# Kernel optimization log

Hardware: AMD Instinct MI355X
Metric: run time of the kernel (lower is better)

## Reference

```python
import jax, jax.numpy as jnp
import numpy as np

N, K, D, H, F = 4, 2048, 512, 8, 2048
Dh = D // H  # per-head dim_q = dim_v = dim_out = 64
EPS = 1e-10


def _uinit(k, shape, fan_sum):
    c = (6.0 / fan_sum) ** 0.5
    return jax.random.uniform(k, shape, jnp.float32, -c, c)


def setup_inputs() -> dict:
    key = jax.random.key(0)
    ks = jax.random.split(key, 8)
    x = jax.random.normal(ks[0], (N, K, D), jnp.float32)
    # per-head projection weights, stacked over heads: (H, D, Dh)
    Wq = _uinit(ks[1], (H, D, Dh), D + Dh)
    Wk = _uinit(ks[2], (H, D, Dh), D + Dh)
    Wv = _uinit(ks[3], (H, D, Dh), D + Dh)
    bq = jnp.zeros((H, Dh), jnp.float32)
    bk = jnp.zeros((H, Dh), jnp.float32)
    bv = jnp.zeros((H, Dh), jnp.float32)
    Wo = _uinit(ks[4], (H * Dh, D), H * Dh + D)
    bo = jnp.zeros((D,), jnp.float32)
    W1 = _uinit(ks[5], (D, F), D + F)
    b1 = jnp.zeros((F,), jnp.float32)
    W2 = _uinit(ks[6], (F, D), F + D)
    b2 = jnp.zeros((D,), jnp.float32)
    g1 = jnp.ones((D,), jnp.float32)
    be1 = jnp.zeros((D,), jnp.float32)
    g2 = jnp.ones((D,), jnp.float32)
    be2 = jnp.zeros((D,), jnp.float32)
    # causal mask: True = masked position (masked_fill semantics)
    mask = jnp.broadcast_to(jnp.triu(jnp.ones((K, K), bool), 1), (N, K, K))
    return dict(x=x, Wq=Wq, bq=bq, Wk=Wk, bk=bk, Wv=Wv, bv=bv, Wo=Wo, bo=bo,
                W1=W1, b1=b1, W2=W2, b2=b2, g1=g1, be1=be1, g2=g2, be2=be2,
                mask=mask)


def _layer_norm(x, g, b):
    m = x.mean(-1, keepdims=True)
    v = ((x - m) ** 2).mean(-1, keepdims=True)
    return g * (x - m) / jnp.sqrt(v + EPS) + b


def _block(x, Wq, bq, Wk, bk, Wv, bv, Wo, bo, W1, b1, W2, b2, g1, be1, g2, be2, mask):
    # per-head projections: (N, H, K, Dh)
    q = jnp.einsum('nkd,hde->nhke', x, Wq) + bq[None, :, None, :]
    k = jnp.einsum('nkd,hde->nhke', x, Wk) + bk[None, :, None, :]
    v = jnp.einsum('nkd,hde->nhke', x, Wv) + bv[None, :, None, :]
    # full score matrix (N, H, K, K) -- faithful to bmm-softmax-bmm
    s = jnp.einsum('nhqe,nhke->nhqk', q, k) / (Dh ** 0.5)
    s = jnp.where(mask[:, None], -1e9, s)
    w = jax.nn.softmax(s, axis=-1)
    att = jnp.einsum('nhqk,nhke->nhqe', w, v)
    att = att.transpose(0, 2, 1, 3).reshape(N, K, H * Dh)  # concat heads
    att = att @ Wo + bo
    h1 = _layer_norm(x + att, g1, be1)
    ff = jax.nn.relu(h1 @ W1 + b1) @ W2 + b2
    return _layer_norm(h1 + ff, g2, be2)


def reference(x, Wq, bq, Wk, bk, Wv, bv, Wo, bo, W1, b1, W2, b2, g1, be1, g2, be2, mask):
    return _block(x, Wq, bq, Wk, bk, Wv, bv, Wo, bo, W1, b1, W2, b2, g1, be1, g2, be2, mask)
```

## Files before the change

### kernel.cpp

```cpp
#include <hip/hip_runtime.h>
#include <cstdint>

typedef unsigned short u16;
typedef __bf16 bf16x8 __attribute__((ext_vector_type(8)));
typedef float f32x4 __attribute__((ext_vector_type(4)));
struct __align__(8) U2 { unsigned x, y; };

#define NEG_INF (-__builtin_inff())

__device__ __forceinline__ u16 f2bf(float f) {
  unsigned u = __builtin_bit_cast(unsigned, f);
  u += 0x7FFFu + ((u >> 16) & 1u);
  return (u16)(u >> 16);
}
__device__ __forceinline__ float bf2f(u16 b) {
  unsigned u = (unsigned)b << 16;
  return __builtin_bit_cast(float, u);
}
__device__ __forceinline__ u16 bfbits(__bf16 x) { return __builtin_bit_cast(u16, x); }
__device__ __forceinline__ unsigned pk2(float a, float b) {
  u16 lo = bfbits((__bf16)a), hi = bfbits((__bf16)b);
  return (unsigned)lo | ((unsigned)hi << 16);
}

__device__ __forceinline__ void async16(u16* dst, const u16* src) {
  __builtin_amdgcn_global_load_lds(
      (__attribute__((address_space(1))) void*)(u16*)src,
      (__attribute__((address_space(3))) void*)dst, 16, 0, 0);
}

__global__ __launch_bounds__(256) void k_cvt(const float4* __restrict__ in,
                                             uint4* __restrict__ out, int n8) {
  int i = blockIdx.x * 256 + threadIdx.x;
  if (i >= n8) return;
  float4 a = in[2 * i], b = in[2 * i + 1];
  uint4 r;
  r.x = (unsigned)f2bf(a.x) | ((unsigned)f2bf(a.y) << 16);
  r.y = (unsigned)f2bf(a.z) | ((unsigned)f2bf(a.w) << 16);
  r.z = (unsigned)f2bf(b.x) | ((unsigned)f2bf(b.y) << 16);
  r.w = (unsigned)f2bf(b.z) | ((unsigned)f2bf(b.w) << 16);
  out[i] = r;
}

__global__ __launch_bounds__(256) void k_prep(const float* __restrict__ Wo,
                                              const float* __restrict__ W1,
                                              const float* __restrict__ W2,
                                              const float* __restrict__ Wq,
                                              const float* __restrict__ Wk,
                                              const float* __restrict__ Wv,
                                              const float* __restrict__ bq,
                                              const float* __restrict__ bk,
                                              const float* __restrict__ bv,
                                              u16* __restrict__ WoT,
                                              u16* __restrict__ W1T,
                                              u16* __restrict__ W2T,
                                              u16* __restrict__ WqkvT,
                                              float* __restrict__ bqkv) {
  const int b = blockIdx.x, tid = threadIdx.x;
  if (b >= 1536) {
    int i = (b - 1536) * 256 + tid;
    int m = i >> 9, r = i & 511;
    const float* B = (m == 0) ? bq : (m == 1) ? bk : bv;
    bqkv[i] = B[r];
    return;
  }
  __shared__ float t[32][65];
  const float* ip;
  u16* op;
  int R, C, r0, c0;
  if (b < 128)      { ip = Wo; op = WoT; R = 512;  C = 512;  c0 = (b & 7) * 64;          r0 = (b >> 3) * 32; }
  else if (b < 640) { int i = b - 128; ip = W1; op = W1T; R = 512;  C = 2048; c0 = (i & 31) * 64; r0 = (i >> 5) * 32; }
  else if (b < 1152){ int i = b - 640; ip = W2; op = W2T; R = 2048; C = 512;  c0 = (i & 7) * 64;  r0 = (i >> 3) * 32; }
  else {
    int i = b - 1152;
    int z = i >> 4;
    const float* W = (z < 8) ? Wq : (z < 16) ? Wk : Wv;
    ip = W + (size_t)(z & 7) * 32768;
    op = WqkvT + (size_t)z * 32768;
    R = 512; C = 64; c0 = 0; r0 = (i & 15) * 32;
  }
  int tx = tid & 63, ty = tid >> 6;
#pragma unroll
  for (int i = 0; i < 32; i += 4)
    t[ty + i][tx] = ip[(size_t)(r0 + ty + i) * C + c0 + tx];
  __syncthreads();
  int cx = tid & 31, cy = tid >> 5;
#pragma unroll
  for (int j = 0; j < 64; j += 8)
    op[(size_t)(c0 + cy + j) * R + r0 + cx] = f2bf(t[cx][cy + j]);
}

template <bool DBUF, int EPI, int BN>
__global__ __launch_bounds__(256) void k_gemm(const u16* __restrict__ A,
                                              const u16* __restrict__ BT,
                                              const float* __restrict__ bias,
                                              u16* __restrict__ Cout,
                                              int M, int N, int Kd) {
  constexpr int HALF = 8192 + BN * 64;
  __shared__ __align__(16) u16 lds[DBUF ? 2 * HALF : HALF];
  constexpr int NFR = BN / 32;
  constexpr int BITER = BN / 32;
  const int tid = threadIdx.x, wid = tid >> 6, lane = tid & 63;
  const int lr = lane & 15, lg = lane >> 4;
  const int wr = wid >> 1, wc = wid & 1;
  const int bid = blockIdx.x;
  const int xcd = bid & 7, local = bid >> 3;
  const int tm = (xcd * 8 + (local & 7)) * 128;
  const int tn = (local >> 3) * BN;

  f32x4 acc[4][NFR] = {};

  const int srow = lane >> 3;
  const int kb = (lane & 7) ^ srow;

  auto STAGE = [&](int buf, int kt) {
    u16* base = lds + buf * HALF;
#pragma unroll
    for (int it = 0; it < 4; ++it) {
      int rid = wid * 4 + it;
      int row = rid * 8 + srow;
      async16(base + rid * 512, A + (size_t)(tm + row) * Kd + kt + kb * 8);
    }
#pragma unroll
    for (int it = 0; it < BITER; ++it) {
      int rid = wid * BITER + it;
      int row = rid * 8 + srow;
      async16(base + 8192 + rid * 512, BT + (size_t)(tn + row) * Kd + kt + kb * 8);
    }
  };

  auto COMPUTE = [&](const char* lp) {
#pragma unroll
    for (int ks = 0; ks < 2; ++ks) {
      const int kbyte = ks * 64 + lg * 16;
      bf16x8 af[4], bfr[NFR];
#pragma unroll
      for (int mi = 0; mi < 4; ++mi) {
        int row = wr * 64 + mi * 16 + lr;
        af[mi] = *(const bf16x8*)(lp + row * 128 + (kbyte ^ ((row & 7) << 4)));
      }
#pragma unroll
      for (int nj = 0; nj < NFR; ++nj) {
        int row = wc * (BN / 2) + nj * 16 + lr;
        bfr[nj] = *(const bf16x8*)(lp + 16384 + row * 128 + (kbyte ^ ((row & 7) << 4)));
      }
#pragma unroll
      for (int mi = 0; mi < 4; ++mi)
#pragma unroll
        for (int nj = 0; nj < NFR; ++nj)
          acc[mi][nj] = __builtin_amdgcn_mfma_f32_16x16x32_bf16(af[mi], bfr[nj], acc[mi][nj], 0, 0, 0);
    }
  };

  const int nkt = Kd >> 6;
  if constexpr (DBUF) {
    STAGE(0, 0);
    for (int ki = 0; ki < nkt; ++ki) {
      __builtin_amdgcn_s_barrier();
      if (ki + 1 < nkt) {
        STAGE((ki + 1) & 1, (ki + 1) << 6);
        if constexpr (BN == 128) asm volatile("s_waitcnt vmcnt(8)" ::: "memory");
        else                     asm volatile("s_waitcnt vmcnt(6)" ::: "memory");
      } else {
        asm volatile("s_waitcnt vmcnt(0)" ::: "memory");
      }
      __builtin_amdgcn_s_barrier();
      __builtin_amdgcn_sched_barrier(0);
      COMPUTE((const char*)(lds + (ki & 1) * HALF));
    }
  } else {
    for (int ki = 0; ki < nkt; ++ki) {
      STAGE(0, ki << 6);
      __syncthreads();
      COMPUTE((const char*)lds);
      __syncthreads();
    }
  }

#pragma unroll
  for (int mi = 0; mi < 4; ++mi)
#pragma unroll
    for (int nj = 0; nj < NFR; ++nj) {
      int col = tn + wc * (BN / 2) + nj * 16 + lr;
      float bv = bias[col];
#pragma unroll
      for (int r = 0; r < 4; ++r) {
        int row = tm + wr * 64 + mi * 16 + lg * 4 + r;
        float v = acc[mi][nj][r] + bv;
        if (EPI == 1) v = v > 0.f ? v : 0.f;
        Cout[(size_t)row * N + col] = f2bf(v);
      }
    }
}

__global__ __launch_bounds__(256) void k_attn(const u16* __restrict__ QKV,
                                              u16* __restrict__ att) {
  __shared__ __align__(16) u16 lds[36864];
  const int lin = blockIdx.x;
  const int L = (lin & 7) * 64 + (lin >> 3);
  const int p = L & 15, nh = L >> 4;
  const int n = nh >> 3, h = nh & 7;
  const int tid = threadIdx.x, wid = tid >> 6, lane = tid & 63;
  const int lr = lane & 15, lg = lane >> 4;
  char* lp = (char*)lds;
  const u16* Qp = QKV + (size_t)(n * 2048) * 1536 + h * 64;
  const u16* Kp = Qp + 512;
  const u16* Vp = Qp + 1024;

  const int vkv = (tid & 31) * 2;
  const int vd0 = (tid >> 5) * 8;
  const int pwb = 65536 + wid * 2048;
  const float C2 = 0.18033688011112042f;
  const float B0 = 14.426950408889634f;

  for (int ph = 0; ph < 2; ++ph) {
    const int qc = (ph == 0) ? p : 31 - p;
    const int ntiles = qc + 1;
    const int qw = qc * 64 + wid * 16;
    const int qa = qw + lr;

    bf16x8 qf[2];
#pragma unroll
    for (int ks = 0; ks < 2; ++ks)
      qf[ks] = *(const bf16x8*)(Qp + (size_t)(qw + lr) * 1536 + ks * 32 + lg * 8);

    f32x4 o[4] = {};
    float lpart = 0.f;

    auto STAGE_K = [&](int t, int b) {
      const int kv0 = t * 64;
#pragma unroll
      for (int it = 0; it < 2; ++it) {
        int c = (wid * 2 + it) * 64 + lane;
        int row = c >> 3, ce = ((c & 7) ^ (row & 7)) * 8;
        async16(&lds[b * 4096 + (wid * 2 + it) * 512],
                Kp + (size_t)(kv0 + row) * 1536 + ce);
      }
    };
    auto VLAND = [&](bf16x8 va, bf16x8 vb, int b) {
#pragma unroll
      for (int jj = 0; jj < 8; ++jj) {
        int d = vd0 + jj;
        unsigned pk = (unsigned)bfbits(va[jj]) | ((unsigned)bfbits(vb[jj]) << 16);
        *(unsigned*)(lp + 32768 + b * 8192 + d * 128 + ((vkv * 2) ^ ((d & 7) << 4))) = pk;
      }
    };
    auto COMPUTE = [&](int t, int b) {
      const int kv0 = t * 64;
      f32x4 s[4] = {};
      __builtin_amdgcn_s_setprio(1);
#pragma unroll
      for (int nj = 0; nj < 4; ++nj) {
        int row = nj * 16 + lr;
#pragma unroll
        for (int ks = 0; ks < 2; ++ks) {
          bf16x8 kf = *(const bf16x8*)(lp + b * 8192 + row * 128 +
                                       ((ks * 64 + lg * 16) ^ ((row & 7) << 4)));
          s[nj] = __builtin_amdgcn_mfma_f32_16x16x32_bf16(kf, qf[ks], s[nj], 0, 0, 0);
        }
      }
      __builtin_amdgcn_s_setprio(0);

      if (t == ntiles - 1) {
#pragma unroll
        for (int nj = 0; nj < 4; ++nj) {
          int kvb = kv0 + nj * 16 + lg * 4;
#pragma unroll
          for (int r = 0; r < 4; ++r)
            if (kvb + r > qa) s[nj][r] = NEG_INF;
        }
      }

      float psum = 0.f;
#pragma unroll
      for (int nj = 0; nj < 4; ++nj)
#pragma unroll
        for (int r = 0; r < 4; ++r) {
          float pv = exp2f(fmaf(s[nj][r], C2, -B0));
          s[nj][r] = pv;
          psum += pv;
        }
      lpart += psum;

#pragma unroll
      for (int nj = 0; nj < 4; ++nj) {
        U2 val;
        val.x = pk2(s[nj][0], s[nj][1]);
        val.y = pk2(s[nj][2], s[nj][3]);
        *(U2*)(lp + pwb + lr * 128 + ((nj * 32 + lg * 8) ^ ((lr & 7) << 4))) = val;
      }

      bf16x8 pa[2];
#pragma unroll
      for (int ks = 0; ks < 2; ++ks)
        pa[ks] = *(const bf16x8*)(lp + pwb + lr * 128 +
                                  ((ks * 64 + lg * 16) ^ ((lr & 7) << 4)));
      __builtin_amdgcn_s_setprio(1);
#pragma unroll
      for (int nd = 0; nd < 4; ++nd) {
        int row = nd * 16 + lr;
#pragma unroll
        for (int ks = 0; ks < 2; ++ks) {
          bf16x8 vf = *(const bf16x8*)(lp + 32768 + b * 8192 + row * 128 +
                                       ((ks * 64 + lg * 16) ^ ((row & 7) << 4)));
          o[nd] = __builtin_amdgcn_mfma_f32_16x16x32_bf16(vf, pa[ks], o[nd], 0, 0, 0);
        }
      }
      __builtin_amdgcn_s_setprio(0);
    };

    STAGE_K(0, 0);
    if (ntiles > 1) STAGE_K(1, 1);
    {
      bf16x8 v0 = *(const bf16x8*)(Vp + (size_t)vkv * 1536 + vd0);
      bf16x8 v1 = *(const bf16x8*)(Vp + (size_t)(vkv + 1) * 1536 + vd0);
      VLAND(v0, v1, 0);
      if (ntiles > 1) {
        bf16x8 v2 = *(const bf16x8*)(Vp + (size_t)(64 + vkv) * 1536 + vd0);
        bf16x8 v3 = *(const bf16x8*)(Vp + (size_t)(64 + vkv + 1) * 1536 + vd0);
        VLAND(v2, v3, 1);
      }
    }
    __syncthreads();

    for (int t = 0; t < ntiles; t += 2) {
      const bool pre0 = (t + 2 < ntiles);
      const bool pre1 = (t + 3 < ntiles);
      bf16x8 va0, vb0, va1, vb1;
      if (pre0) {
        STAGE_K(t + 2, (t + 2) & 3);
        va0 = *(const bf16x8*)(Vp + (size_t)((t + 2) * 64 + vkv) * 1536 + vd0);
        vb0 = *(const bf16x8*)(Vp + (size_t)((t + 2) * 64 + vkv + 1) * 1536 + vd0);
      }
      if (pre1) {
        STAGE_K(t + 3, (t + 3) & 3);
        va1 = *(const bf16x8*)(Vp + (size_t)((t + 3) * 64 + vkv) * 1536 + vd0);
        vb1 = *(const bf16x8*)(Vp + (size_t)((t + 3) * 64 + vkv + 1) * 1536 + vd0);
      }

      COMPUTE(t, t & 3);
      if (t + 1 < ntiles) COMPUTE(t + 1, (t + 1) & 3);

      if (pre0) VLAND(va0, vb0, (t + 2) & 3);
      if (pre1) VLAND(va1, vb1, (t + 3) & 3);
      __syncthreads();
    }

    float lsum = lpart;
    lsum += __shfl_xor(lsum, 16);
    lsum += __shfl_xor(lsum, 32);
    float li = 1.0f / lsum;

    u16* ap = att + (size_t)(n * 2048 + qw + lr) * 512 + h * 64 + lg * 4;
#pragma unroll
    for (int nd = 0; nd < 4; ++nd) {
      U2 val;
      val.x = pk2(o[nd][0] * li, o[nd][1] * li);
      val.y = pk2(o[nd][2] * li, o[nd][3] * li);
      *(U2*)(ap + nd * 16) = val;
    }
  }
}

template <bool XF32>
__global__ __launch_bounds__(256) void k_add_ln(const void* __restrict__ Xp,
                                                const u16* __restrict__ Yb,
                                                const float* __restrict__ gam,
                                                const float* __restrict__ bet,
                                                float* __restrict__ outf,
                                                u16* __restrict__ outb) {
  const int wid = threadIdx.x >> 6, lane = threadIdx.x & 63;
  const size_t row = (size_t)blockIdx.x * 4 + wid;
  float xv[8];
  if constexpr (XF32) {
    const float4* x = (const float4*)((const float*)Xp + row * 512);
    float4 a0 = x[lane], a1 = x[lane + 64];
    xv[0] = a0.x; xv[1] = a0.y; xv[2] = a0.z; xv[3] = a0.w;
    xv[4] = a1.x; xv[5] = a1.y; xv[6] = a1.z; xv[7] = a1.w;
  } else {
    const u16* x = (const u16*)Xp + row * 512;
    U2 x0 = *(const U2*)(x + lane * 4);
    U2 x1 = *(const U2*)(x + 256 + lane * 4);
    xv[0] = bf2f((u16)(x0.x & 0xFFFF)); xv[1] = bf2f((u16)(x0.x >> 16));
    xv[2] = bf2f((u16)(x0.y & 0xFFFF)); xv[3] = bf2f((u16)(x0.y >> 16));
    xv[4] = bf2f((u16)(x1.x & 0xFFFF)); xv[5] = bf2f((u16)(x1.x >> 16));
    xv[6] = bf2f((u16)(x1.y & 0xFFFF)); xv[7] = bf2f((u16)(x1.y >> 16));
  }
  U2 y0 = *(const U2*)(Yb + row * 512 + lane * 4);
  U2 y1 = *(const U2*)(Yb + row * 512 + 256 + lane * 4);
  float v[8];
  v[0] = xv[0] + bf2f((u16)(y0.x & 0xFFFF));
  v[1] = xv[1] + bf2f((u16)(y0.x >> 16));
  v[2] = xv[2] + bf2f((u16)(y0.y & 0xFFFF));
  v[3] = xv[3] + bf2f((u16)(y0.y >> 16));
  v[4] = xv[4] + bf2f((u16)(y1.x & 0xFFFF));
  v[5] = xv[5] + bf2f((u16)(y1.x >> 16));
  v[6] = xv[6] + bf2f((u16)(y1.y & 0xFFFF));
  v[7] = xv[7] + bf2f((u16)(y1.y >> 16));
  float s = 0.f, ss = 0.f;
#pragma unroll
  for (int i = 0; i < 8; ++i) { s += v[i]; ss += v[i] * v[i]; }
#pragma unroll
  for (int m = 1; m < 64; m <<= 1) { s += __shfl_xor(s, m); ss += __shfl_xor(ss, m); }
  float mean = s * (1.f / 512.f);
  float var = ss * (1.f / 512.f) - mean * mean;
  float rstd = rsqrtf(var + 1e-10f);
  float4 g0 = ((const float4*)gam)[lane], g1 = ((const float4*)gam)[lane + 64];
  float4 e0 = ((const float4*)bet)[lane], e1 = ((const float4*)bet)[lane + 64];
  float o[8];
  o[0] = g0.x * (v[0] - mean) * rstd + e0.x;
  o[1] = g0.y * (v[1] - mean) * rstd + e0.y;
  o[2] = g0.z * (v[2] - mean) * rstd + e0.z;
  o[3] = g0.w * (v[3] - mean) * rstd + e0.w;
  o[4] = g1.x * (v[4] - mean) * rstd + e1.x;
  o[5] = g1.y * (v[5] - mean) * rstd + e1.y;
  o[6] = g1.z * (v[6] - mean) * rstd + e1.z;
  o[7] = g1.w * (v[7] - mean) * rstd + e1.w;
  if (outf) {
    float4* of = (float4*)(outf + row * 512);
    float4 w0, w1;
    w0.x = o[0]; w0.y = o[1]; w0.z = o[2]; w0.w = o[3];
    w1.x = o[4]; w1.y = o[5]; w1.z = o[6]; w1.w = o[7];
    of[lane] = w0;
    of[lane + 64] = w1;
  }
  if (outb) {
    u16* ob = outb + row * 512;
    U2 p0, p1;
    p0.x = pk2(o[0], o[1]); p0.y = pk2(o[2], o[3]);
    p1.x = pk2(o[4], o[5]); p1.y = pk2(o[6], o[7]);
    *(U2*)(ob + lane * 4) = p0;
    *(U2*)(ob + 256 + lane * 4) = p1;
  }
}

extern "C" void kernel_launch(void* const* d_in, const int* in_sizes, int n_in,
                              void* d_out, int out_size, void* d_ws, size_t ws_size,
                              hipStream_t stream) {
  const float* x  = (const float*)d_in[0];
  const float* Wq = (const float*)d_in[1];
  const float* bq = (const float*)d_in[2];
  const float* Wk = (const float*)d_in[3];
  const float* bk = (const float*)d_in[4];
  const float* Wv = (const float*)d_in[5];
  const float* bv = (const float*)d_in[6];
  const float* Wo = (const float*)d_in[7];
  const float* bo = (const float*)d_in[8];
  const float* W1 = (const float*)d_in[9];
  const float* b1 = (const float*)d_in[10];
  const float* W2 = (const float*)d_in[11];
  const float* b2 = (const float*)d_in[12];
  const float* g1 = (const float*)d_in[13];
  const float* be1 = (const float*)d_in[14];
  const float* g2 = (const float*)d_in[15];
  const float* be2 = (const float*)d_in[16];

  char* ws = (char*)d_ws;
  u16* xb   = (u16*)(ws + 0);
  u16* attb = (u16*)(ws + 0);
  u16* h1b  = (u16*)(ws + 0);
  u16* WqkvT = (u16*)(ws + (size_t)(8u << 20));
  u16* WoT = WqkvT + 786432;
  u16* W1T = WoT + 262144;
  u16* W2T = W1T + 1048576;
  float* bqkv = (float*)(W2T + 1048576);
  u16* QKV = (u16*)(ws + (size_t)(16u << 20));
  u16* attproj = (u16*)(ws + (size_t)(16u << 20));
  u16* ff1 = (u16*)(ws + (size_t)(16u << 20));
  u16* ffn2 = (u16*)(ws + (size_t)(50u << 20));

  k_cvt<<<2048, 256, 0, stream>>>((const float4*)x, (uint4*)xb, 524288);
  k_prep<<<1542, 256, 0, stream>>>(Wo, W1, W2, Wq, Wk, Wv, bq, bk, bv,
                                   WoT, W1T, W2T, WqkvT, bqkv);

  k_gemm<true, 0, 128><<<768, 256, 0, stream>>>(xb, WqkvT, bqkv, QKV, 8192, 1536, 512);
  k_attn<<<512, 256, 0, stream>>>(QKV, attb);
  k_gemm<true, 0, 64><<<512, 256, 0, stream>>>(attb, WoT, bo, attproj, 8192, 512, 512);
  k_add_ln<true><<<2048, 256, 0, stream>>>(x, attproj, g1, be1, nullptr, h1b);
  k_gemm<false, 1, 128><<<1024, 256, 0, stream>>>(h1b, W1T, b1, ff1, 8192, 2048, 512);
  k_gemm<true, 0, 64><<<512, 256, 0, stream>>>(ff1, W2T, b2, ffn2, 8192, 512, 2048);
  k_add_ln<false><<<2048, 256, 0, stream>>>(h1b, ffn2, g2, be2, (float*)d_out, nullptr);
}
```

Before: 158.5 us.

## Load K fragments directly from global into registers, drop K LDS staging

K tiles are no longer staged through LDS with async copies. Each wave now loads its MFMA K fragments straight from global memory into registers, double-buffered one tile ahead, and the LDS footprint shrinks to hold only V and P. This removes the LDS write/read traffic for K and the smaller LDS allocation may allow more blocks per CU. The cost is higher register pressure and redundant global loads of K across the four waves, which now rely on cache hits.

```diff
diff --git a/kernel.cpp b/kernel.cpp
--- a/kernel.cpp
+++ b/kernel.cpp
@@ -195,7 +195,7 @@
 
 __global__ __launch_bounds__(256) void k_attn(const u16* __restrict__ QKV,
                                               u16* __restrict__ att) {
-  __shared__ __align__(16) u16 lds[36864];
+  __shared__ __align__(16) u16 lds[20480];
   const int lin = blockIdx.x;
   const int L = (lin & 7) * 64 + (lin >> 3);
   const int p = L & 15, nh = L >> 4;
@@ -209,9 +209,10 @@
 
   const int vkv = (tid & 31) * 2;
   const int vd0 = (tid >> 5) * 8;
-  const int pwb = 65536 + wid * 2048;
+  const int pwb = 32768 + wid * 2048;
   const float C2 = 0.18033688011112042f;
   const float B0 = 14.426950408889634f;
+  const u16* Kfb = Kp + (size_t)lr * 1536 + lg * 8;
 
   for (int ph = 0; ph < 2; ++ph) {
     const int qc = (ph == 0) ? p : 31 - p;
@@ -226,39 +227,35 @@
 
     f32x4 o[4] = {};
     float lpart = 0.f;
-
-    auto STAGE_K = [&](int t, int b) {
-      const int kv0 = t * 64;
-#pragma unroll
-      for (int it = 0; it < 2; ++it) {
-        int c = (wid * 2 + it) * 64 + lane;
-        int row = c >> 3, ce = ((c & 7) ^ (row & 7)) * 8;
-        async16(&lds[b * 4096 + (wid * 2 + it) * 512],
-                Kp + (size_t)(kv0 + row) * 1536 + ce);
-      }
+    bf16x8 kfA[4][2], kfB[4][2];
+
+    auto KLOAD = [&](bf16x8 (&kf)[4][2], int t) {
+      const size_t base = (size_t)(t * 64) * 1536;
+#pragma unroll
+      for (int nj = 0; nj < 4; ++nj)
+#pragma unroll
+        for (int ks = 0; ks < 2; ++ks)
+          kf[nj][ks] = *(const bf16x8*)(Kfb + base + (size_t)(nj * 16) * 1536 + ks * 32);
     };
     auto VLAND = [&](bf16x8 va, bf16x8 vb, int b) {
 #pragma unroll
       for (int jj = 0; jj < 8; ++jj) {
         int d = vd0 + jj;
         unsigned pk = (unsigned)bfbits(va[jj]) | ((unsigned)bfbits(vb[jj]) << 16);
-        *(unsigned*)(lp + 32768 + b * 8192 + d * 128 + ((vkv * 2) ^ ((d & 7) << 4))) = pk;
+        *(unsigned*)(lp + b * 8192 + d * 128 + ((vkv * 2) ^ ((d & 7) << 4))) = pk;
       }
     };
-    auto COMPUTE = [&](int t, int b) {
+    auto TILE = [&](bf16x8 (&kfc)[4][2], bf16x8 (&kfn)[4][2], int t) {
+      if (t + 1 < ntiles) KLOAD(kfn, t + 1);
+
       const int kv0 = t * 64;
       f32x4 s[4] = {};
       __builtin_amdgcn_s_setprio(1);
 #pragma unroll
-      for (int nj = 0; nj < 4; ++nj) {
-        int row = nj * 16 + lr;
-#pragma unroll
-        for (int ks = 0; ks < 2; ++ks) {
-          bf16x8 kf = *(const bf16x8*)(lp + b * 8192 + row * 128 +
-                                       ((ks * 64 + lg * 16) ^ ((row & 7) << 4)));
-          s[nj] = __builtin_amdgcn_mfma_f32_16x16x32_bf16(kf, qf[ks], s[nj], 0, 0, 0);
-        }
-      }
+      for (int nj = 0; nj < 4; ++nj)
+#pragma unroll
+        for (int ks = 0; ks < 2; ++ks)
+          s[nj] = __builtin_amdgcn_mfma_f32_16x16x32_bf16(kfc[nj][ks], qf[ks], s[nj], 0, 0, 0);
       __builtin_amdgcn_s_setprio(0);
 
       if (t == ntiles - 1) {
@@ -301,7 +298,7 @@
         int row = nd * 16 + lr;
 #pragma unroll
         for (int ks = 0; ks < 2; ++ks) {
-          bf16x8 vf = *(const bf16x8*)(lp + 32768 + b * 8192 + row * 128 +
+          bf16x8 vf = *(const bf16x8*)(lp + (t & 3) * 8192 + row * 128 +
                                        ((ks * 64 + lg * 16) ^ ((row & 7) << 4)));
           o[nd] = __builtin_amdgcn_mfma_f32_16x16x32_bf16(vf, pa[ks], o[nd], 0, 0, 0);
         }
@@ -309,8 +306,7 @@
       __builtin_amdgcn_s_setprio(0);
     };
 
-    STAGE_K(0, 0);
-    if (ntiles > 1) STAGE_K(1, 1);
+    KLOAD(kfA, 0);
     {
       bf16x8 v0 = *(const bf16x8*)(Vp + (size_t)vkv * 1536 + vd0);
       bf16x8 v1 = *(const bf16x8*)(Vp + (size_t)(vkv + 1) * 1536 + vd0);
@@ -328,18 +324,16 @@
       const bool pre1 = (t + 3 < ntiles);
       bf16x8 va0, vb0, va1, vb1;
       if (pre0) {
-        STAGE_K(t + 2, (t + 2) & 3);
         va0 = *(const bf16x8*)(Vp + (size_t)((t + 2) * 64 + vkv) * 1536 + vd0);
         vb0 = *(const bf16x8*)(Vp + (size_t)((t + 2) * 64 + vkv + 1) * 1536 + vd0);
       }
       if (pre1) {
-        STAGE_K(t + 3, (t + 3) & 3);
         va1 = *(const bf16x8*)(Vp + (size_t)((t + 3) * 64 + vkv) * 1536 + vd0);
         vb1 = *(const bf16x8*)(Vp + (size_t)((t + 3) * 64 + vkv + 1) * 1536 + vd0);
       }
 
-      COMPUTE(t, t & 3);
-      if (t + 1 < ntiles) COMPUTE(t + 1, (t + 1) & 3);
+      TILE(kfA, kfB, t);
+      if (t + 1 < ntiles) TILE(kfB, kfA, t + 1);
 
       if (pre0) VLAND(va0, vb0, (t + 2) & 3);
       if (pre1) VLAND(va1, vb1, (t + 3) & 3);
```

New measurement: 189.5 us. 19.6% more time.
